# Kernel optimization log

Hardware: AMD Instinct MI355X
Metric: run time of the kernel (lower is better)

## Reference

```python
import jax, jax.numpy as jnp
import numpy as np

C = 256          # in_channels == inter_channels (structurally required)
B, H, W = 16, 64, 64


def setup_inputs() -> dict:
    key = jax.random.key(0)
    ks = jax.random.split(key, 10)
    s = 1.0 / np.sqrt(C)
    x = jax.random.normal(ks[0], (B, C, H, W), dtype=jnp.float32)
    # theta / phi: 1x1 convs, stored as [out, in]
    theta_w = jax.random.normal(ks[1], (C, C), dtype=jnp.float32) * s
    theta_b = jax.random.normal(ks[2], (C,), dtype=jnp.float32) * s
    phi_w = jax.random.normal(ks[3], (C, C), dtype=jnp.float32) * s
    phi_b = jax.random.normal(ks[4], (C,), dtype=jnp.float32) * s
    # grouped conv: Conv2d(C, 2C, kernel=(C,1), groups=C).
    # torch weight [2C, 1, C, 1] with group-major out-channel order -> [C groups, 2 per group, C taps]
    gw = jax.random.normal(ks[5], (C, 2, C), dtype=jnp.float32) * s
    gb = jax.random.normal(ks[6], (C, 2), dtype=jnp.float32) * s
    # dim_adjust: 1x1 conv 2C -> C, stored as [C, 2C]
    dw = jax.random.normal(ks[7], (C, 2 * C), dtype=jnp.float32) * (1.0 / np.sqrt(2 * C))
    db = jax.random.normal(ks[8], (C,), dtype=jnp.float32) * (1.0 / np.sqrt(2 * C))
    return {"x": x, "theta_w": theta_w, "theta_b": theta_b,
            "phi_w": phi_w, "phi_b": phi_b,
            "gw": gw, "gb": gb, "dw": dw, "db": db}


def reference(x, theta_w, theta_b, phi_w, phi_b, gw, gb, dw, db):
    b, c, h, w = x.shape
    xf = x.reshape(b, c, h * w)                                   # [B,C,HW]
    theta = jnp.einsum('oc,bcn->bon', theta_w, xf) + theta_b[:, None]  # [B,Ci,HW]
    phi = jnp.einsum('oc,bcn->bon', phi_w, xf) + phi_b[:, None]        # [B,Ci,HW]
    f = jnp.einsum('bon,bpn->bop', theta, phi)                    # [B,Ci,Ci] channel similarity
    # grouped conv: group g sees channel g of f over its 'spatial' axis (length Ci),
    # producing 2 outputs per group via a full-height dot product.
    g = jnp.einsum('bgk,gjk->bgj', f, gw) + gb                    # [B,C,2]
    g = jax.nn.relu(g).reshape(b, 2 * c)                          # [B,2C]
    out = jnp.einsum('bo,co->bc', g, dw) + db                     # [B,C] 1x1 conv
    return out[:, :, None, None]                                  # [B,C,1,1]
```

## Files before the change

### kernel.cpp

```cpp
#include <hip/hip_runtime.h>


#define CC  256
#define NB  16
#define HWN 4096
#define KSPLIT 32
#define NPAIR 136

typedef __attribute__((ext_vector_type(4))) float f32x4;
typedef __attribute__((ext_vector_type(8))) short bf16x8;

__device__ inline unsigned short f2bf(float f) {
  unsigned u = __float_as_uint(f);
  u += 0x7fff + ((u >> 16) & 1);
  return (unsigned short)(u >> 16);
}
__device__ inline float bf2f(unsigned u) { return __uint_as_float(u << 16); }

__global__ __launch_bounds__(1024, 4) void k_gram(const float* __restrict__ x,
                                                  unsigned short* __restrict__ slab,
                                                  float* __restrict__ Spart,
                                                  const float* __restrict__ gw,
                                                  const float* __restrict__ pw,
                                                  const float* __restrict__ pb,
                                                  unsigned short* __restrict__ Qh,
                                                  float* __restrict__ E) {
  __shared__ __align__(16) unsigned short As[2][256 * 64];
  const int blk = blockIdx.x, tid = threadIdx.x;

  if (blk < 128) {
    const int sub = tid >> 8, t = tid & 255;
    const int rj = blk * 4 + sub;
    float* smg = (float*)As + sub * 640;
    smg[t] = gw[rj * 256 + t];
    __syncthreads();
    float q0 = 0.f, q1 = 0.f, q2 = 0.f, q3 = 0.f;
    #pragma unroll 4
    for (int o = 0; o < 256; o += 4) {
      q0 += smg[o]     * pw[o * 256 + t];
      q1 += smg[o + 1] * pw[(o + 1) * 256 + t];
      q2 += smg[o + 2] * pw[(o + 2) * 256 + t];
      q3 += smg[o + 3] * pw[(o + 3) * 256 + t];
    }
    Qh[rj * 256 + t] = f2bf((q0 + q1) + (q2 + q3));
    float e = smg[t] * pb[t];
    e += __shfl_xor(e, 1);
    e += __shfl_xor(e, 2);
    e += __shfl_xor(e, 4);
    e += __shfl_xor(e, 8);
    e += __shfl_xor(e, 16);
    e += __shfl_xor(e, 32);
    if ((t & 63) == 0) smg[512 + (t >> 6)] = e;
    __syncthreads();
    if (t == 0) E[rj] = smg[512] + smg[513] + smg[514] + smg[515];
    return;
  }

  const int gblk = blk - 128;
  const int ks = gblk >> 4, b = gblk & 15;
  const float* xb = x + (size_t)b * CC * HWN;

  const int w = tid >> 6, lane = tid & 63;
  const int quad = lane >> 4, m15 = lane & 15;
  const int srow = tid >> 4;
  const int scol = (tid & 15) << 2;
  const int sg = scol >> 3, so = scol & 7;

  f32x4 acc[16];
  #pragma unroll
  for (int i = 0; i < 16; ++i) acc[i] = (f32x4){0.f, 0.f, 0.f, 0.f};
  float rs[4] = {0.f, 0.f, 0.f, 0.f};

  const int k0 = ks * 128;
  float4 ld[4];
  #pragma unroll
  for (int p = 0; p < 4; ++p)
    ld[p] = *(const float4*)(xb + (size_t)(p * 64 + srow) * HWN + k0 + scol);
  #pragma unroll
  for (int p = 0; p < 4; ++p) {
    const int row = p * 64 + srow;
    rs[p] += ld[p].x + ld[p].y + ld[p].z + ld[p].w;
    *(ushort4*)&As[0][row * 64 + ((sg ^ (row & 7)) << 3) + so] =
        make_ushort4(f2bf(ld[p].x), f2bf(ld[p].y), f2bf(ld[p].z), f2bf(ld[p].w));
  }
  __syncthreads();

  #pragma unroll
  for (int i = 0; i < 2; ++i) {
    if (i < 1) {
      #pragma unroll
      for (int p = 0; p < 4; ++p)
        ld[p] = *(const float4*)(xb + (size_t)(p * 64 + srow) * HWN + k0 + 64 + scol);
    }
    const int rowa = 16 * w + m15;
    #pragma unroll
    for (int kkg = 0; kkg < 8; kkg += 4) {
      const int ga = (kkg + quad) ^ (m15 & 7);
      bf16x8 af = *(const bf16x8*)&As[i][rowa * 64 + ga * 8];
      #pragma unroll
      for (int ct = 0; ct < 16; ++ct) {
        if (ct < w) continue;
        bf16x8 bfr = *(const bf16x8*)&As[i][(16 * ct + m15) * 64 + ga * 8];
        acc[ct] = __builtin_amdgcn_mfma_f32_16x16x32_bf16(af, bfr, acc[ct], 0, 0, 0);
      }
    }
    if (i < 1) {
      #pragma unroll
      for (int p = 0; p < 4; ++p) {
        const int row = p * 64 + srow;
        rs[p] += ld[p].x + ld[p].y + ld[p].z + ld[p].w;
        *(ushort4*)&As[1][row * 64 + ((sg ^ (row & 7)) << 3) + so] =
            make_ushort4(f2bf(ld[p].x), f2bf(ld[p].y), f2bf(ld[p].z), f2bf(ld[p].w));
      }
    }
    __syncthreads();
  }

  const int off_w = 16 * w - (w * (w - 1)) / 2;
  unsigned short* sbase = slab + ((size_t)(ks * 16 + b) * NPAIR) * 256;
  #pragma unroll
  for (int ct = 0; ct < 16; ++ct) {
    if (ct < w) continue;
    const int pid = off_w + (ct - w);
    uint2 ov;
    ov.x = (unsigned)f2bf(acc[ct][0]) | ((unsigned)f2bf(acc[ct][1]) << 16);
    ov.y = (unsigned)f2bf(acc[ct][2]) | ((unsigned)f2bf(acc[ct][3]) << 16);
    *(uint2*)(sbase + pid * 256 + lane * 4) = ov;
  }

  #pragma unroll
  for (int p = 0; p < 4; ++p) {
    float v = rs[p];
    v += __shfl_xor(v, 1);
    v += __shfl_xor(v, 2);
    v += __shfl_xor(v, 4);
    v += __shfl_xor(v, 8);
    if ((tid & 15) == 0)
      Spart[(ks * 16 + b) * 256 + p * 64 + srow] = v;
  }
}

__global__ __launch_bounds__(256) void k_fuse2(const unsigned short* __restrict__ slab,
                                               const float* __restrict__ Spart,
                                               const float* __restrict__ pw,
                                               const float* __restrict__ tw,
                                               const float* __restrict__ db,
                                               unsigned short* __restrict__ Gh,
                                               float* __restrict__ U,
                                               float* __restrict__ V,
                                               float* __restrict__ out) {
  const int blk = blockIdx.x, tid = threadIdx.x;
  if (blk < 544) {
    const int t = blk * 256 + tid;
    const int b = t / 8704;
    const int rem = t % 8704;
    const int pid0 = rem >> 6, lane = rem & 63;
    int w = 0, p = pid0;
    while (p >= 16 - w) { p -= 16 - w; ++w; }
    const int ct = w + p;
    const int quad = lane >> 4, m15 = lane & 15;
    float s[4] = {0.f, 0.f, 0.f, 0.f};
    const unsigned short* sp = slab + (size_t)(b * NPAIR + pid0) * 256 + lane * 4;
    #pragma unroll
    for (int ks = 0; ks < KSPLIT; ++ks) {
      const uint2 v = *(const uint2*)(sp + (size_t)ks * 16 * NPAIR * 256);
      s[0] += bf2f(v.x & 0xffffu); s[1] += bf2f(v.x >> 16);
      s[2] += bf2f(v.y & 0xffffu); s[3] += bf2f(v.y >> 16);
    }
    unsigned short h[4];
    #pragma unroll
    for (int r = 0; r < 4; ++r) h[r] = f2bf(s[r]);
    unsigned short* Gb = Gh + ((size_t)b << 16);
    const int rb = 16 * w + quad * 4;
    const int col = 16 * ct + m15;
    #pragma unroll
    for (int r = 0; r < 4; ++r) Gb[(rb + r) * 256 + col] = h[r];
    uint2 mv;
    mv.x = (unsigned)h[0] | ((unsigned)h[1] << 16);
    mv.y = (unsigned)h[2] | ((unsigned)h[3] << 16);
    *(uint2*)(Gb + col * 256 + rb) = mv;
  } else if (blk < 576) {
    const int m = blk - 544;
    const int b = m & 15, mat = m >> 4;
    const float* Wm = mat ? pw : tw;
    float* outp = mat ? V : U;
    __shared__ float sm[256];
    float sv = 0.f;
    #pragma unroll
    for (int ks = 0; ks < KSPLIT; ++ks)
      sv += Spart[(ks * 16 + b) * 256 + tid];
    sm[tid] = sv;
    __syncthreads();
    const int l = tid & 15, oh = tid >> 4;
    #pragma unroll
    for (int oc = 0; oc < 16; ++oc) {
      const int o = oc * 16 + oh;
      float a = 0.f;
      #pragma unroll
      for (int j = 0; j < 16; ++j)
        a += Wm[o * 256 + l * 16 + j] * sm[l * 16 + j];
      a += __shfl_xor(a, 1);
      a += __shfl_xor(a, 2);
      a += __shfl_xor(a, 4);
      a += __shfl_xor(a, 8);
      if (l == 0) outp[b * 256 + o] = a;
    }
  } else {
    const int b = blk - 576;
    out[b * 256 + tid] = db[tid];
  }
}

__global__ __launch_bounds__(256) void k_p(const unsigned short* __restrict__ Gh,
                                           const unsigned short* __restrict__ Qh,
                                           const float* __restrict__ tw,
                                           const float* __restrict__ gw,
                                           const float* __restrict__ U,
                                           const float* __restrict__ V,
                                           const float* __restrict__ E,
                                           const float* __restrict__ tb,
                                           const float* __restrict__ gb,
                                           const float* __restrict__ dw,
                                           float* __restrict__ out) {
  const int rjt = blockIdx.x, b = blockIdx.y;
  const int rj0 = rjt * 16;
  const int tid = threadIdx.x, w = tid >> 6, lane = tid & 63;
  const int quad = lane >> 4, m15 = lane & 15;
  const unsigned short* Gb = Gh + ((size_t)b << 16);

  f32x4 acc[4];
  #pragma unroll
  for (int mt = 0; mt < 4; ++mt) acc[mt] = (f32x4){0.f, 0.f, 0.f, 0.f};

  #pragma unroll
  for (int s = 0; s < 8; ++s) {
    const int kb = s * 32 + quad * 8;
    bf16x8 bq = *(const bf16x8*)(Qh + (rj0 + m15) * 256 + kb);
    #pragma unroll
    for (int mt = 0; mt < 4; ++mt) {
      bf16x8 ag = *(const bf16x8*)(Gb + (64 * w + 16 * mt + m15) * 256 + kb);
      acc[mt] = __builtin_amdgcn_mfma_f32_16x16x32_bf16(ag, bq, acc[mt], 0, 0, 0);
    }
  }

  __shared__ float sred[16 * 4];
  __shared__ float sred2[16];
  __shared__ float gsh[16];
  {
    const int rj = rj0 + m15;
    const int r = rj >> 1;
    float p = 0.f;
    #pragma unroll
    for (int mt = 0; mt < 4; ++mt)
      #pragma unroll
      for (int reg = 0; reg < 4; ++reg)
        p += acc[mt][reg] * tw[r * 256 + 64 * w + 16 * mt + quad * 4 + reg];
    p += __shfl_xor(p, 16);
    p += __shfl_xor(p, 32);
    if (quad == 0) sred[m15 * 4 + w] = p;
  }
  {
    const int oi = tid >> 4, seg = tid & 15;
    const int rj = rj0 + oi;
    float p2 = 0.f;
    #pragma unroll
    for (int i = 0; i < 16; ++i) {
      const int cp = seg * 16 + i;
      p2 += gw[rj * 256 + cp] * V[b * 256 + cp];
    }
    p2 += __shfl_xor(p2, 1);
    p2 += __shfl_xor(p2, 2);
    p2 += __shfl_xor(p2, 4);
    p2 += __shfl_xor(p2, 8);
    if (seg == 0) sred2[oi] = p2;
  }
  __syncthreads();
  if (tid < 16) {
    const int rj = rj0 + tid, r = rj >> 1;
    const float v = sred[tid * 4] + sred[tid * 4 + 1] +
                    sred[tid * 4 + 2] + sred[tid * 4 + 3];
    const float tbr = tb[r];
    const float bias = tbr * sred2[tid] +
                       (U[b * 256 + r] + 4096.0f * tbr) * E[rj] + gb[rj];
    gsh[tid] = fmaxf(v + bias, 0.f);
  }
  __syncthreads();
  float a = 0.f;
  #pragma unroll
  for (int i = 0; i < 16; ++i)
    a += gsh[i] * dw[tid * 512 + rj0 + i];
  atomicAdd(&out[b * 256 + tid], a);
}

extern "C" void kernel_launch(void* const* d_in, const int* in_sizes, int n_in,
                              void* d_out, int out_size, void* d_ws, size_t ws_size,
                              hipStream_t stream) {
  const float* x  = (const float*)d_in[0];
  const float* tw = (const float*)d_in[1];
  const float* tb = (const float*)d_in[2];
  const float* pw = (const float*)d_in[3];
  const float* pb = (const float*)d_in[4];
  const float* gw = (const float*)d_in[5];
  const float* gb = (const float*)d_in[6];
  const float* dw = (const float*)d_in[7];
  const float* db = (const float*)d_in[8];
  float* out = (float*)d_out;

  unsigned short* slab = (unsigned short*)d_ws;
  unsigned short* Gh   = slab + (size_t)KSPLIT * 16 * NPAIR * 256;
  unsigned short* Qh   = Gh + ((size_t)16 << 16);
  float* Spart = (float*)(Qh + 512 * 256);
  float* E  = Spart + KSPLIT * 16 * 256;
  float* U  = E + 512;
  float* V  = U + NB * 256;

  k_gram<<<640, 1024, 0, stream>>>(x, slab, Spart, gw, pw, pb, Qh, E);
  k_fuse2<<<592, 256, 0, stream>>>(slab, Spart, pw, tw, db, Gh, U, V, out);
  k_p<<<dim3(32, NB), 256, 0, stream>>>(Gh, Qh, tw, gw, U, V, E, tb, gb, dw, out);
}
```

Before: 154.2 us.

## Halve K-split of Gram kernel and move Q/E precompute into fuse kernel

```diff
diff --git a/kernel.cpp b/kernel.cpp
--- a/kernel.cpp
+++ b/kernel.cpp
@@ -4,7 +4,7 @@
 #define CC  256
 #define NB  16
 #define HWN 4096
-#define KSPLIT 32
+#define KSPLIT 16
 #define NPAIR 136
 
 typedef __attribute__((ext_vector_type(4))) float f32x4;
@@ -19,45 +19,10 @@
 
 __global__ __launch_bounds__(1024, 4) void k_gram(const float* __restrict__ x,
                                                   unsigned short* __restrict__ slab,
-                                                  float* __restrict__ Spart,
-                                                  const float* __restrict__ gw,
-                                                  const float* __restrict__ pw,
-                                                  const float* __restrict__ pb,
-                                                  unsigned short* __restrict__ Qh,
-                                                  float* __restrict__ E) {
+                                                  float* __restrict__ Spart) {
   __shared__ __align__(16) unsigned short As[2][256 * 64];
   const int blk = blockIdx.x, tid = threadIdx.x;
-
-  if (blk < 128) {
-    const int sub = tid >> 8, t = tid & 255;
-    const int rj = blk * 4 + sub;
-    float* smg = (float*)As + sub * 640;
-    smg[t] = gw[rj * 256 + t];
-    __syncthreads();
-    float q0 = 0.f, q1 = 0.f, q2 = 0.f, q3 = 0.f;
-    #pragma unroll 4
-    for (int o = 0; o < 256; o += 4) {
-      q0 += smg[o]     * pw[o * 256 + t];
-      q1 += smg[o + 1] * pw[(o + 1) * 256 + t];
-      q2 += smg[o + 2] * pw[(o + 2) * 256 + t];
-      q3 += smg[o + 3] * pw[(o + 3) * 256 + t];
-    }
-    Qh[rj * 256 + t] = f2bf((q0 + q1) + (q2 + q3));
-    float e = smg[t] * pb[t];
-    e += __shfl_xor(e, 1);
-    e += __shfl_xor(e, 2);
-    e += __shfl_xor(e, 4);
-    e += __shfl_xor(e, 8);
-    e += __shfl_xor(e, 16);
-    e += __shfl_xor(e, 32);
-    if ((t & 63) == 0) smg[512 + (t >> 6)] = e;
-    __syncthreads();
-    if (t == 0) E[rj] = smg[512] + smg[513] + smg[514] + smg[515];
-    return;
-  }
-
-  const int gblk = blk - 128;
-  const int ks = gblk >> 4, b = gblk & 15;
+  const int ks = blk >> 4, b = blk & 15;
   const float* xb = x + (size_t)b * CC * HWN;
 
   const int w = tid >> 6, lane = tid & 63;
@@ -71,7 +36,7 @@
   for (int i = 0; i < 16; ++i) acc[i] = (f32x4){0.f, 0.f, 0.f, 0.f};
   float rs[4] = {0.f, 0.f, 0.f, 0.f};
 
-  const int k0 = ks * 128;
+  const int k0 = ks * 256;
   float4 ld[4];
   #pragma unroll
   for (int p = 0; p < 4; ++p)
@@ -86,30 +51,32 @@
   __syncthreads();
 
   #pragma unroll
-  for (int i = 0; i < 2; ++i) {
-    if (i < 1) {
+  for (int i = 0; i < 4; ++i) {
+    const int cur = i & 1;
+    if (i < 3) {
+      const int kc = k0 + (i + 1) * 64;
       #pragma unroll
       for (int p = 0; p < 4; ++p)
-        ld[p] = *(const float4*)(xb + (size_t)(p * 64 + srow) * HWN + k0 + 64 + scol);
+        ld[p] = *(const float4*)(xb + (size_t)(p * 64 + srow) * HWN + kc + scol);
     }
     const int rowa = 16 * w + m15;
     #pragma unroll
     for (int kkg = 0; kkg < 8; kkg += 4) {
       const int ga = (kkg + quad) ^ (m15 & 7);
-      bf16x8 af = *(const bf16x8*)&As[i][rowa * 64 + ga * 8];
+      bf16x8 af = *(const bf16x8*)&As[cur][rowa * 64 + ga * 8];
       #pragma unroll
       for (int ct = 0; ct < 16; ++ct) {
         if (ct < w) continue;
-        bf16x8 bfr = *(const bf16x8*)&As[i][(16 * ct + m15) * 64 + ga * 8];
+        bf16x8 bfr = *(const bf16x8*)&As[cur][(16 * ct + m15) * 64 + ga * 8];
         acc[ct] = __builtin_amdgcn_mfma_f32_16x16x32_bf16(af, bfr, acc[ct], 0, 0, 0);
       }
     }
-    if (i < 1) {
+    if (i < 3) {
       #pragma unroll
       for (int p = 0; p < 4; ++p) {
         const int row = p * 64 + srow;
         rs[p] += ld[p].x + ld[p].y + ld[p].z + ld[p].w;
-        *(ushort4*)&As[1][row * 64 + ((sg ^ (row & 7)) << 3) + so] =
+        *(ushort4*)&As[1 - cur][row * 64 + ((sg ^ (row & 7)) << 3) + so] =
             make_ushort4(f2bf(ld[p].x), f2bf(ld[p].y), f2bf(ld[p].z), f2bf(ld[p].w));
       }
     }
@@ -142,10 +109,14 @@
 
 __global__ __launch_bounds__(256) void k_fuse2(const unsigned short* __restrict__ slab,
                                                const float* __restrict__ Spart,
+                                               const float* __restrict__ gw,
                                                const float* __restrict__ pw,
+                                               const float* __restrict__ pb,
                                                const float* __restrict__ tw,
                                                const float* __restrict__ db,
                                                unsigned short* __restrict__ Gh,
+                                               unsigned short* __restrict__ Qh,
+                                               float* __restrict__ E,
                                                float* __restrict__ U,
                                                float* __restrict__ V,
                                                float* __restrict__ out) {
@@ -179,8 +150,32 @@
     mv.x = (unsigned)h[0] | ((unsigned)h[1] << 16);
     mv.y = (unsigned)h[2] | ((unsigned)h[3] << 16);
     *(uint2*)(Gb + col * 256 + rb) = mv;
-  } else if (blk < 576) {
-    const int m = blk - 544;
+  } else if (blk < 1056) {
+    const int rj = blk - 544;
+    __shared__ float smg[260];
+    smg[tid] = gw[rj * 256 + tid];
+    __syncthreads();
+    float q0 = 0.f, q1 = 0.f, q2 = 0.f, q3 = 0.f;
+    #pragma unroll 4
+    for (int o = 0; o < 256; o += 4) {
+      q0 += smg[o]     * pw[o * 256 + tid];
+      q1 += smg[o + 1] * pw[(o + 1) * 256 + tid];
+      q2 += smg[o + 2] * pw[(o + 2) * 256 + tid];
+      q3 += smg[o + 3] * pw[(o + 3) * 256 + tid];
+    }
+    Qh[rj * 256 + tid] = f2bf((q0 + q1) + (q2 + q3));
+    float e = smg[tid] * pb[tid];
+    e += __shfl_xor(e, 1);
+    e += __shfl_xor(e, 2);
+    e += __shfl_xor(e, 4);
+    e += __shfl_xor(e, 8);
+    e += __shfl_xor(e, 16);
+    e += __shfl_xor(e, 32);
+    if ((tid & 63) == 0) smg[256 + (tid >> 6)] = e;
+    __syncthreads();
+    if (tid == 0) E[rj] = smg[256] + smg[257] + smg[258] + smg[259];
+  } else if (blk < 1088) {
+    const int m = blk - 1056;
     const int b = m & 15, mat = m >> 4;
     const float* Wm = mat ? pw : tw;
     float* outp = mat ? V : U;
@@ -206,7 +201,7 @@
       if (l == 0) outp[b * 256 + o] = a;
     }
   } else {
-    const int b = blk - 576;
+    const int b = blk - 1088;
     out[b * 256 + tid] = db[tid];
   }
 }
@@ -314,7 +309,8 @@
   float* U  = E + 512;
   float* V  = U + NB * 256;
 
-  k_gram<<<640, 1024, 0, stream>>>(x, slab, Spart, gw, pw, pb, Qh, E);
-  k_fuse2<<<592, 256, 0, stream>>>(slab, Spart, pw, tw, db, Gh, U, V, out);
+  k_gram<<<256, 1024, 0, stream>>>(x, slab, Spart);
+  k_fuse2<<<1104, 256, 0, stream>>>(slab, Spart, gw, pw, pb, tw, db,
+                                    Gh, Qh, E, U, V, out);
   k_p<<<dim3(32, NB), 256, 0, stream>>>(Gh, Qh, tw, gw, U, V, E, tb, gb, dw, out);
 }
```

Result: faster. 147.6 us (median of 2 runs) (-4.3%).
